# Optimization experiments

Measured on AMD Instinct MI355X. Metric: run time of the kernel, lower is better.

Reference implementation:

```python
import jax, jax.numpy as jnp
import numpy as np

B, L, NMOD = 200, 50, 3          # dialogues, uniform dialogue length, modalities (l,a,v)
N_DIM, NHIDDEN, NUM_K, NSPK = 128, 128, 4, 2
NN = B * NMOD * L                # total graph nodes = 30000


def _build_edge_index():
    # within-modality full permutations per dialogue
    idx = np.arange(L)
    u, v = np.meshgrid(idx, idx, indexing='ij')
    m = u != v
    pw = np.stack([u[m], v[m]])                                    # [2, L*(L-1)]
    offs = (np.arange(B)[:, None] * NMOD * L + np.arange(NMOD)[None, :] * L).reshape(-1)
    within = (pw[None, :, :] + offs[:, None, None]).transpose(1, 0, 2).reshape(2, -1)
    # cross-modal permutations of (l_t, a_t, v_t) per utterance
    mo = np.arange(NMOD) * L
    mu, mv = np.meshgrid(mo, mo, indexing='ij')
    mm = mu != mv
    pc = np.stack([mu[mm], mv[mm]])                                # [2, 6]
    offs2 = (np.arange(B)[:, None] * NMOD * L + np.arange(L)[None, :]).reshape(-1)
    cross = (pc[None, :, :] + offs2[:, None, None]).transpose(1, 0, 2).reshape(2, -1)
    return np.concatenate([within, cross], axis=1).astype(np.int32)  # [2, 1530000]


def setup_inputs():
    key = jax.random.key(0)
    ks = jax.random.split(key, 6)
    a = jax.random.normal(ks[0], (B * L, N_DIM), jnp.float32)
    v = jax.random.normal(ks[1], (B * L, N_DIM), jnp.float32)
    l = jax.random.normal(ks[2], (B * L, N_DIM), jnp.float32)
    qmask = jax.random.uniform(ks[3], (L, B, NSPK), jnp.float32)
    W1 = jax.random.normal(ks[4], (NHIDDEN, N_DIM), jnp.float32) / np.sqrt(N_DIM)
    b1 = jnp.zeros((NHIDDEN,), jnp.float32)
    speaker_emb = jax.random.normal(ks[5], (NSPK, N_DIM), jnp.float32)
    kappas = jnp.ones((NUM_K,), jnp.float32)
    edge_index = jnp.asarray(_build_edge_index())
    return {"a": a, "v": v, "l": l, "qmask": qmask, "W1": W1, "b1": b1,
            "speaker_emb": speaker_emb, "kappas": kappas,
            "edge_index": edge_index, "epoch": 0}


def _hgcn_block(x, src, dst, inv_deg, kappa):
    # gather-aggregate-scatter hypergraph conv: mean over incoming edges, kappa-weighted residual
    agg = jax.ops.segment_sum(x[src], dst, num_segments=NN) * inv_deg
    return jax.nn.relu(x + kappa * agg)


def reference(a, v, l, qmask, W1, b1, speaker_emb, kappas, edge_index, epoch):
    # flatten qmask per dialogue (uniform lengths) -> speaker id per utterance
    spk_idx = jnp.argmax(qmask.transpose(1, 0, 2).reshape(B * L, NSPK), axis=-1)
    l = l + speaker_emb[spk_idx]                    # use_speaker and 'l' in modals
    # per-dialogue node ordering: [l_b; a_b; v_b]
    feats = jnp.concatenate([l.reshape(B, L, N_DIM),
                             a.reshape(B, L, N_DIM),
                             v.reshape(B, L, N_DIM)], axis=1).reshape(NN, N_DIM)
    x = feats @ W1.T + b1
    src, dst = edge_index[0], edge_index[1]
    deg = jax.ops.segment_sum(jnp.ones((src.shape[0],), jnp.float32), dst, num_segments=NN)
    inv_deg = (1.0 / jnp.maximum(deg, 1.0))[:, None]
    for k in range(NUM_K):
        x = _hgcn_block(x, src, dst, inv_deg, kappas[k])
    x = jnp.concatenate([feats, x], axis=-1)        # use_residue
    D = x.shape[-1]
    xr = x.reshape(B, NMOD, L, D)
    # reverse_features: cat l/a/v feature blocks along last dim, utterance-major
    out = jnp.concatenate([xr[:, 0], xr[:, 1], xr[:, 2]], axis=-1).reshape(B * L, NMOD * D)
    return out
```

## Files before the change

### kernel.cpp

```cpp
#include <hip/hip_runtime.h>

#define NB   200
#define LL   50
#define ND   128
#define NROW 150

typedef __attribute__((ext_vector_type(8))) short bf16x8;
typedef __attribute__((ext_vector_type(4))) float f32x4;

#define FS   136
#define SMEM_BYTES 155136

__device__ __forceinline__ int XADDR(int row, int c) {
    return row * 128 + (((c) ^ (row & 7)) << 2);
}

__device__ __forceinline__ short f2bf(float x) {
    unsigned u = __float_as_uint(x);
    return (short)((u + 0x7fffu + ((u >> 16) & 1u)) >> 16);
}

__device__ __forceinline__ float bf2f(short h) {
    return __uint_as_float(((unsigned)(unsigned short)h) << 16);
}

__device__ __forceinline__ bf16x8 pack8(f32x4 lo, f32x4 hi) {
    bf16x8 r;
    r[0] = f2bf(lo[0]); r[1] = f2bf(lo[1]); r[2] = f2bf(lo[2]); r[3] = f2bf(lo[3]);
    r[4] = f2bf(hi[0]); r[5] = f2bf(hi[1]); r[6] = f2bf(hi[2]); r[7] = f2bf(hi[3]);
    return r;
}

__launch_bounds__(1024, 4)
__global__ void hgcn_fused(const float* __restrict__ a,
                           const float* __restrict__ v,
                           const float* __restrict__ l,
                           const float* __restrict__ qmask,
                           const float* __restrict__ W1,
                           const float* __restrict__ b1,
                           const float* __restrict__ se,
                           const float* __restrict__ kap,
                           float* __restrict__ out) {
    extern __shared__ char smem[];
    short* featsB = (short*)smem;
    short* Wlds   = (short*)(smem + 43520);
    float* xbuf   = (float*)(smem + 78336);

    const int b    = blockIdx.x;
    const int tid  = threadIdx.x;
    const int lane = tid & 63;
    const int w2   = tid >> 6;

    const f32x4* a4  = (const f32x4*)a;
    const f32x4* v4  = (const f32x4*)v;
    const f32x4* l4  = (const f32x4*)l;
    const f32x4* se4 = (const f32x4*)se;
    const f32x4* W14 = (const f32x4*)W1;
    f32x4* out4 = (f32x4*)out;

    const f32x4 kap4 = *(const f32x4*)kap;

    for (int i = tid; i < 2560; i += 1024) {
        int row = i >> 4, c8 = i & 15;
        f32x4 f0 = {0.f, 0.f, 0.f, 0.f}, f1 = {0.f, 0.f, 0.f, 0.f};
        if (row < NROW) {
            int m = row >= 100 ? 2 : (row >= 50 ? 1 : 0);
            int t = row - m * 50;
            const f32x4* src = (m == 0) ? l4 : ((m == 1) ? a4 : v4);
            int base = (b * LL + t) * 32 + c8 * 2;
            f0 = src[base]; f1 = src[base + 1];
            if (m == 0) {
                int qb  = (t * NB + b) * 2;
                int spk = qmask[qb + 1] > qmask[qb] ? 1 : 0;
                f0 += se4[spk * 32 + c8 * 2];
                f1 += se4[spk * 32 + c8 * 2 + 1];
            }
        }
        *(bf16x8*)&featsB[row * FS + c8 * 8] = pack8(f0, f1);
    }
    for (int i = tid; i < 2048; i += 1024) {
        int row = i >> 4, c8 = i & 15;
        f32x4 f0 = W14[row * 32 + c8 * 2];
        f32x4 f1 = W14[row * 32 + c8 * 2 + 1];
        *(bf16x8*)&Wlds[row * FS + c8 * 8] = pack8(f0, f1);
    }
    __syncthreads();

    {
        const int dt = w2 & 7;
        const int ng = w2 >> 3;
        const int r  = lane & 15;
        const int q  = lane >> 4;
        f32x4 bias = *(const f32x4*)&b1[16 * dt + 4 * q];
        bf16x8 afr[4];
        #pragma unroll
        for (int ks = 0; ks < 4; ++ks)
            afr[ks] = *(const bf16x8*)&Wlds[(16 * dt + r) * FS + ks * 32 + q * 8];
        #pragma unroll
        for (int nt = ng; nt < 10; nt += 2) {
            f32x4 acc = {0.f, 0.f, 0.f, 0.f};
            #pragma unroll
            for (int ks = 0; ks < 4; ++ks) {
                bf16x8 bfr = *(const bf16x8*)&featsB[(16 * nt + r) * FS + ks * 32 + q * 8];
                acc = __builtin_amdgcn_mfma_f32_16x16x32_bf16(afr[ks], bfr, acc, 0, 0, 0);
            }
            int node = 16 * nt + r;
            if (node < NROW)
                *(f32x4*)&xbuf[XADDR(node, 4 * dt + q)] = acc + bias;
        }
    }
    __syncthreads();

    if (tid < 512) {
        const int w8   = tid >> 6;
        const int dlow = lane & 15;
        const int tg   = lane >> 4;
        const int d    = w8 * 16 + dlow;
        const int c4   = d >> 2, e4 = d & 3;

        float x[3][13];
        #pragma unroll
        for (int m = 0; m < 3; ++m)
            #pragma unroll
            for (int j = 0; j < 13; ++j) {
                int t = tg * 13 + j;
                float val = 0.0f;
                if (t < LL) {
                    int row = m * 50 + t;
                    val = xbuf[row * 128 + (((c4 ^ (row & 7)) << 2) | e4)];
                }
                x[m][j] = val;
            }

        const float inv = 1.0f / 51.0f;
        #pragma unroll
        for (int it = 0; it < 4; ++it) {
            const float f = kap4[it] * inv;
            float S[3];
            #pragma unroll
            for (int m = 0; m < 3; ++m) {
                float s = 0.0f;
                #pragma unroll
                for (int j = 0; j < 13; ++j) s += x[m][j];
                s += __shfl_xor(s, 16, 64);
                s += __shfl_xor(s, 32, 64);
                S[m] = s;
            }
            #pragma unroll
            for (int j = 0; j < 13; ++j) {
                bool valid = (tg * 13 + j) < LL;
                float c = x[0][j] + x[1][j] + x[2][j];
                #pragma unroll
                for (int m = 0; m < 3; ++m) {
                    float sc = S[m] + c;
                    float r  = fmaxf(fmaf(f, sc - 2.0f * x[m][j], x[m][j]), 0.0f);
                    x[m][j] = valid ? r : 0.0f;
                }
            }
        }

        #pragma unroll
        for (int m = 0; m < 3; ++m)
            #pragma unroll
            for (int j = 0; j < 13; ++j) {
                int t = tg * 13 + j;
                if (t < LL)
                    out[(size_t)(b * LL + t) * 768 + m * 256 + 128 + d] = x[m][j];
            }
    } else {
        for (int i = tid - 512; i < 2400; i += 512) {
            int row = i >> 4, c8 = i & 15;
            int m = row >= 100 ? 2 : (row >= 50 ? 1 : 0);
            int t = row - m * 50;
            bf16x8 hv = *(const bf16x8*)&featsB[row * FS + c8 * 8];
            f32x4 f0, f1;
            f0[0] = bf2f(hv[0]); f0[1] = bf2f(hv[1]); f0[2] = bf2f(hv[2]); f0[3] = bf2f(hv[3]);
            f1[0] = bf2f(hv[4]); f1[1] = bf2f(hv[5]); f1[2] = bf2f(hv[6]); f1[3] = bf2f(hv[7]);
            size_t o = (size_t)(b * LL + t) * 192 + m * 64 + c8 * 2;
            out4[o]     = f0;
            out4[o + 1] = f1;
        }
    }
}

extern "C" void kernel_launch(void* const* d_in, const int* in_sizes, int n_in,
                              void* d_out, int out_size, void* d_ws, size_t ws_size,
                              hipStream_t stream) {
    const float* a     = (const float*)d_in[0];
    const float* v     = (const float*)d_in[1];
    const float* l     = (const float*)d_in[2];
    const float* qmask = (const float*)d_in[3];
    const float* W1    = (const float*)d_in[4];
    const float* b1    = (const float*)d_in[5];
    const float* se    = (const float*)d_in[6];
    const float* kap   = (const float*)d_in[7];
    float* out = (float*)d_out;

    hipFuncSetAttribute((const void*)hgcn_fused,
                        hipFuncAttributeMaxDynamicSharedMemorySize, SMEM_BYTES);
    hgcn_fused<<<NB, 1024, SMEM_BYTES, stream>>>(a, v, l, qmask, W1, b1, se, kap, out);
}
```

Baseline: 18.00 us.

## Keep GEMM accumulators in registers for graph iterations, drop LDS staging buffer

The block shrinks to 512 threads. Each wave now owns 16 output features and computes all 12 node tiles, holding the MFMA results in registers. The 4 hypergraph mean-aggregation iterations then run directly on those accumulators, which removes the xbuf LDS round trip, one barrier and the W1 LDS staging, since W1 fragments are loaded straight from global memory. Rows are padded to 64 per modality so tiles align with modalities, at the cost of some wasted MFMA work on padding, more register pressure, and fewer threads for the load and copy phases.

```diff
diff --git a/kernel.cpp b/kernel.cpp
--- a/kernel.cpp
+++ b/kernel.cpp
@@ -3,17 +3,12 @@
 #define NB   200
 #define LL   50
 #define ND   128
-#define NROW 150
 
 typedef __attribute__((ext_vector_type(8))) short bf16x8;
 typedef __attribute__((ext_vector_type(4))) float f32x4;
 
 #define FS   136
-#define SMEM_BYTES 155136
-
-__device__ __forceinline__ int XADDR(int row, int c) {
-    return row * 128 + (((c) ^ (row & 7)) << 2);
-}
+#define SMEM_BYTES (192 * FS * 2)
 
 __device__ __forceinline__ short f2bf(float x) {
     unsigned u = __float_as_uint(x);
@@ -31,7 +26,7 @@
     return r;
 }
 
-__launch_bounds__(1024, 4)
+__launch_bounds__(512, 2)
 __global__ void hgcn_fused(const float* __restrict__ a,
                            const float* __restrict__ v,
                            const float* __restrict__ l,
@@ -43,13 +38,14 @@
                            float* __restrict__ out) {
     extern __shared__ char smem[];
     short* featsB = (short*)smem;
-    short* Wlds   = (short*)(smem + 43520);
-    float* xbuf   = (float*)(smem + 78336);
 
     const int b    = blockIdx.x;
     const int tid  = threadIdx.x;
     const int lane = tid & 63;
-    const int w2   = tid >> 6;
+    const int w    = tid >> 6;
+    const int r    = lane & 15;
+    const int q    = lane >> 4;
+    const int d    = 16 * w + r;
 
     const f32x4* a4  = (const f32x4*)a;
     const f32x4* v4  = (const f32x4*)v;
@@ -59,13 +55,20 @@
     f32x4* out4 = (f32x4*)out;
 
     const f32x4 kap4 = *(const f32x4*)kap;
+    const float bias = b1[d];
+    bf16x8 wfr[4];
+    #pragma unroll
+    for (int ks = 0; ks < 4; ++ks) {
+        f32x4 g0 = W14[(16 * w + r) * 32 + ks * 8 + q * 2];
+        f32x4 g1 = W14[(16 * w + r) * 32 + ks * 8 + q * 2 + 1];
+        wfr[ks] = pack8(g0, g1);
+    }
 
-    for (int i = tid; i < 2560; i += 1024) {
-        int row = i >> 4, c8 = i & 15;
+    for (int i = tid; i < 3072; i += 512) {
+        int prow = i >> 4, c8 = i & 15;
+        int m = prow >> 6, t = prow & 63;
         f32x4 f0 = {0.f, 0.f, 0.f, 0.f}, f1 = {0.f, 0.f, 0.f, 0.f};
-        if (row < NROW) {
-            int m = row >= 100 ? 2 : (row >= 50 ? 1 : 0);
-            int t = row - m * 50;
+        if (t < LL) {
             const f32x4* src = (m == 0) ? l4 : ((m == 1) ? a4 : v4);
             int base = (b * LL + t) * 32 + c8 * 2;
             f0 = src[base]; f1 = src[base + 1];
@@ -76,103 +79,26 @@
                 f1 += se4[spk * 32 + c8 * 2 + 1];
             }
         }
-        *(bf16x8*)&featsB[row * FS + c8 * 8] = pack8(f0, f1);
-    }
-    for (int i = tid; i < 2048; i += 1024) {
-        int row = i >> 4, c8 = i & 15;
-        f32x4 f0 = W14[row * 32 + c8 * 2];
-        f32x4 f1 = W14[row * 32 + c8 * 2 + 1];
-        *(bf16x8*)&Wlds[row * FS + c8 * 8] = pack8(f0, f1);
+        *(bf16x8*)&featsB[prow * FS + c8 * 8] = pack8(f0, f1);
     }
     __syncthreads();
 
-    {
-        const int dt = w2 & 7;
-        const int ng = w2 >> 3;
-        const int r  = lane & 15;
-        const int q  = lane >> 4;
-        f32x4 bias = *(const f32x4*)&b1[16 * dt + 4 * q];
-        bf16x8 afr[4];
+    f32x4 acc[12];
+    #pragma unroll
+    for (int nt = 0; nt < 12; ++nt) acc[nt] = (f32x4){0.f, 0.f, 0.f, 0.f};
+    #pragma unroll
+    for (int ks = 0; ks < 4; ++ks)
         #pragma unroll
-        for (int ks = 0; ks < 4; ++ks)
-            afr[ks] = *(const bf16x8*)&Wlds[(16 * dt + r) * FS + ks * 32 + q * 8];
-        #pragma unroll
-        for (int nt = ng; nt < 10; nt += 2) {
-            f32x4 acc = {0.f, 0.f, 0.f, 0.f};
-            #pragma unroll
-            for (int ks = 0; ks < 4; ++ks) {
-                bf16x8 bfr = *(const bf16x8*)&featsB[(16 * nt + r) * FS + ks * 32 + q * 8];
-                acc = __builtin_amdgcn_mfma_f32_16x16x32_bf16(afr[ks], bfr, acc, 0, 0, 0);
-            }
-            int node = 16 * nt + r;
-            if (node < NROW)
-                *(f32x4*)&xbuf[XADDR(node, 4 * dt + q)] = acc + bias;
-        }
-    }
-    __syncthreads();
-
-    if (tid < 512) {
-        const int w8   = tid >> 6;
-        const int dlow = lane & 15;
-        const int tg   = lane >> 4;
-        const int d    = w8 * 16 + dlow;
-        const int c4   = d >> 2, e4 = d & 3;
-
-        float x[3][13];
-        #pragma unroll
-        for (int m = 0; m < 3; ++m)
-            #pragma unroll
-            for (int j = 0; j < 13; ++j) {
-                int t = tg * 13 + j;
-                float val = 0.0f;
-                if (t < LL) {
-                    int row = m * 50 + t;
-                    val = xbuf[row * 128 + (((c4 ^ (row & 7)) << 2) | e4)];
-                }
-                x[m][j] = val;
-            }
-
-        const float inv = 1.0f / 51.0f;
-        #pragma unroll
-        for (int it = 0; it < 4; ++it) {
-            const float f = kap4[it] * inv;
-            float S[3];
-            #pragma unroll
-            for (int m = 0; m < 3; ++m) {
-                float s = 0.0f;
-                #pragma unroll
-                for (int j = 0; j < 13; ++j) s += x[m][j];
-                s += __shfl_xor(s, 16, 64);
-                s += __shfl_xor(s, 32, 64);
-                S[m] = s;
-            }
-            #pragma unroll
-            for (int j = 0; j < 13; ++j) {
-                bool valid = (tg * 13 + j) < LL;
-                float c = x[0][j] + x[1][j] + x[2][j];
-                #pragma unroll
-                for (int m = 0; m < 3; ++m) {
-                    float sc = S[m] + c;
-                    float r  = fmaxf(fmaf(f, sc - 2.0f * x[m][j], x[m][j]), 0.0f);
-                    x[m][j] = valid ? r : 0.0f;
-                }
-            }
+        for (int nt = 0; nt < 12; ++nt) {
+            bf16x8 af = *(const bf16x8*)&featsB[(16 * nt + r) * FS + ks * 32 + q * 8];
+            acc[nt] = __builtin_amdgcn_mfma_f32_16x16x32_bf16(af, wfr[ks], acc[nt], 0, 0, 0);
         }
 
-        #pragma unroll
-        for (int m = 0; m < 3; ++m)
-            #pragma unroll
-            for (int j = 0; j < 13; ++j) {
-                int t = tg * 13 + j;
-                if (t < LL)
-                    out[(size_t)(b * LL + t) * 768 + m * 256 + 128 + d] = x[m][j];
-            }
-    } else {
-        for (int i = tid - 512; i < 2400; i += 512) {
-            int row = i >> 4, c8 = i & 15;
-            int m = row >= 100 ? 2 : (row >= 50 ? 1 : 0);
-            int t = row - m * 50;
-            bf16x8 hv = *(const bf16x8*)&featsB[row * FS + c8 * 8];
+    for (int i = tid; i < 3072; i += 512) {
+        int prow = i >> 4, c8 = i & 15;
+        int m = prow >> 6, t = prow & 63;
+        if (t < LL) {
+            bf16x8 hv = *(const bf16x8*)&featsB[prow * FS + c8 * 8];
             f32x4 f0, f1;
             f0[0] = bf2f(hv[0]); f0[1] = bf2f(hv[1]); f0[2] = bf2f(hv[2]); f0[3] = bf2f(hv[3]);
             f1[0] = bf2f(hv[4]); f1[1] = bf2f(hv[5]); f1[2] = bf2f(hv[6]); f1[3] = bf2f(hv[7]);
@@ -181,6 +107,59 @@
             out4[o + 1] = f1;
         }
     }
+
+    #pragma unroll
+    for (int nt = 0; nt < 12; ++nt) {
+        int t0 = 16 * (nt & 3) + 4 * q;
+        #pragma unroll
+        for (int e = 0; e < 4; ++e)
+            acc[nt][e] = (t0 + e < LL) ? acc[nt][e] + bias : 0.0f;
+    }
+
+    const float inv = 1.0f / 51.0f;
+    #pragma unroll
+    for (int it = 0; it < 4; ++it) {
+        const float f = kap4[it] * inv;
+        const float g = 1.0f - 2.0f * f;
+        float S[3];
+        #pragma unroll
+        for (int m = 0; m < 3; ++m) {
+            f32x4 s4 = acc[4 * m] + acc[4 * m + 1] + acc[4 * m + 2] + acc[4 * m + 3];
+            float s = s4[0] + s4[1] + s4[2] + s4[3];
+            s += __shfl_xor(s, 16, 64);
+            s += __shfl_xor(s, 32, 64);
+            S[m] = s;
+        }
+        #pragma unroll
+        for (int j = 0; j < 4; ++j) {
+            int t0 = 16 * j + 4 * q;
+            #pragma unroll
+            for (int e = 0; e < 4; ++e) {
+                float c = acc[j][e] + acc[4 + j][e] + acc[8 + j][e];
+                bool valid = (t0 + e) < LL;
+                #pragma unroll
+                for (int m = 0; m < 3; ++m) {
+                    float xv = acc[4 * m + j][e];
+                    float nv = fmaxf(fmaf(f, S[m] + c, g * xv), 0.0f);
+                    acc[4 * m + j][e] = valid ? nv : 0.0f;
+                }
+            }
+        }
+    }
+
+    const size_t ob = (size_t)b * LL * 768 + 128 + d;
+    #pragma unroll
+    for (int m = 0; m < 3; ++m)
+        #pragma unroll
+        for (int j = 0; j < 4; ++j) {
+            int t0 = 16 * j + 4 * q;
+            #pragma unroll
+            for (int e = 0; e < 4; ++e) {
+                int t = t0 + e;
+                if (t < LL)
+                    out[ob + (size_t)t * 768 + m * 256] = acc[4 * m + j][e];
+            }
+        }
 }
 
 extern "C" void kernel_launch(void* const* d_in, const int* in_sizes, int n_in,
@@ -198,5 +177,5 @@
 
     hipFuncSetAttribute((const void*)hgcn_fused,
                         hipFuncAttributeMaxDynamicSharedMemorySize, SMEM_BYTES);
-    hgcn_fused<<<NB, 1024, SMEM_BYTES, stream>>>(a, v, l, qmask, W1, b1, se, kap, out);
+    hgcn_fused<<<NB, 512, SMEM_BYTES, stream>>>(a, v, l, qmask, W1, b1, se, kap, out);
 }
```

Result: slower. 20.91 us (+16.2%).
